# Optimization experiments

Measured on AMD Instinct MI355X. Metric: run time of the kernel, lower is better.

Reference implementation:

```python
import jax, jax.numpy as jnp
import numpy as np

B, T, C = 2, 1024, 1024
NH, HS, BD, HORIZON = 16, 64, 16, 64


def setup_inputs() -> dict:
    key = jax.random.key(0)
    ks = jax.random.split(key, 16)
    s = 0.02
    return {
        "x": jax.random.normal(ks[0], (B, T, C), jnp.float32),
        "W_disp": jax.random.normal(ks[1], (NH * BD, C), jnp.float32) * s,
        "b_disp": jnp.zeros((NH * BD,), jnp.float32),
        "W_val": jax.random.normal(ks[2], (C, C), jnp.float32) * s,
        "b_val": jnp.zeros((C,), jnp.float32),
        "rel_pos_emb": jax.random.normal(ks[3], (HORIZON, BD), jnp.float32) * s,
        "W_fused": jax.random.normal(ks[4], (2 * BD, BD), jnp.float32) * s,
        "b_fused": jnp.zeros((2 * BD,), jnp.float32),
        "W_pos": jax.random.normal(ks[5], (BD, BD), jnp.float32) * s,
        "W_bond": jax.random.normal(ks[6], (BD,), jnp.float32) * s,
        "b_bond": jnp.zeros((), jnp.float32),
        "W_dmg": jax.random.normal(ks[7], (BD,), jnp.float32) * s,
        "b_dmg": jnp.full((), -3.0, jnp.float32),  # nn.init.constant_(damage_out.bias, -3.0)
        "W_cproj": jax.random.normal(ks[8], (C, C), jnp.float32) * s,
        "b_cproj": jnp.zeros((C,), jnp.float32),
    }


def reference(x, W_disp, b_disp, W_val, b_val, rel_pos_emb, W_fused, b_fused,
              W_pos, W_bond, b_bond, W_dmg, b_dmg, W_cproj, b_cproj):
    delta = min(HORIZON, T)
    gelu = lambda z: jax.nn.gelu(z, approximate=False)  # torch F.gelu default (erf)

    # projections + head split: (B,nh,T,bd) / (B,nh,T,hs)
    disp = (x @ W_disp.T + b_disp).reshape(B, T, NH, BD).transpose(0, 2, 1, 3)
    val = (x @ W_val.T + b_val).reshape(B, T, NH, HS).transpose(0, 2, 1, 3)

    pad = delta - 1
    disp_pad = jnp.pad(disp, ((0, 0), (0, 0), (pad, 0), (0, 0)))
    idx = jnp.arange(T)[:, None] + jnp.arange(delta)[None, :]  # (T,delta) into padded axis
    disp_win = disp_pad[:, :, idx]                      # (B,nh,T,delta,bd)
    strain = disp_win - disp[:, :, :, None, :]          # bond strain

    fused = strain @ W_fused.T + b_fused                # (B,nh,T,delta,2bd)
    bond_f, dmg_f = fused[..., :BD], fused[..., BD:]
    pos_feat = rel_pos_emb[:delta] @ W_pos.T            # (delta,bd)

    bond_logits = gelu(bond_f + pos_feat) @ W_bond + b_bond          # (B,nh,T,delta)
    damage = jax.nn.sigmoid(gelu(dmg_f) @ W_dmg + b_dmg)             # (B,nh,T,delta)
    logits = bond_logits - 10.0 * damage

    cmask = (jnp.arange(T)[:, None] - delta + 1 + jnp.arange(delta)[None, :]) >= 0
    logits = jnp.where(cmask[None, None], logits, -jnp.inf)
    weights = jax.nn.softmax(logits, axis=-1)           # (B,nh,T,delta)

    # weighted sum over window without materializing (B,nh,T,delta,hs)
    val_pad = jnp.pad(val, ((0, 0), (0, 0), (pad, 0), (0, 0)))
    def body(acc, j):
        sl = jax.lax.dynamic_slice_in_dim(val_pad, j, T, axis=2)  # (B,nh,T,hs)
        return acc + weights[..., j][..., None] * sl, None
    out0 = jnp.zeros((B, NH, T, HS), jnp.float32)
    out, _ = jax.lax.scan(body, out0, jnp.arange(delta))

    y = out.transpose(0, 2, 1, 3).reshape(B, T, C)
    return y @ W_cproj.T + b_cproj
```

## Files before the change

### kernel.cpp

```cpp
#include <hip/hip_runtime.h>

#define BDIM 16
#define HSZ 64
#define NHEAD 16
#define DELTA 64
#define LOG2E 1.4426950408889634f

typedef __bf16 bf16x8 __attribute__((ext_vector_type(8)));
typedef float f32x4 __attribute__((ext_vector_type(4)));
typedef float f32x2 __attribute__((ext_vector_type(2)));
typedef unsigned short us8 __attribute__((ext_vector_type(8)));
typedef unsigned int u32;

__device__ __forceinline__ unsigned short f2bf(float f) {
    u32 u = __float_as_uint(f);
    return (unsigned short)((u + 0x7fffu + ((u >> 16) & 1u)) >> 16);
}
__device__ __forceinline__ float bf2f(unsigned short s) {
    return __uint_as_float(((u32)s) << 16);
}

__device__ __forceinline__ void gload_lds16(const void* g, void* l) {
    __builtin_amdgcn_global_load_lds(
        (const __attribute__((address_space(1))) void*)g,
        (__attribute__((address_space(3))) void*)l, 16, 0, 0);
}

__global__ __launch_bounds__(256) void cast4_bf16(
    const float* __restrict__ s0, unsigned short* __restrict__ d0,
    const float* __restrict__ s1, unsigned short* __restrict__ d1,
    const float* __restrict__ s2, unsigned short* __restrict__ d2,
    const float* __restrict__ s3, unsigned short* __restrict__ d3,
    const float* __restrict__ bd, const float* __restrict__ bv,
    float* __restrict__ bcat) {
    int blk = blockIdx.x;
    if (blk == 4352) {
        for (int t = threadIdx.x; t < 320; t += 256) {
            if (t < 64) ((float4*)bcat)[t] = ((const float4*)bd)[t];
            else        ((float4*)bcat)[t] = ((const float4*)bv)[t - 64];
        }
        return;
    }
    const float* src; unsigned short* dst; int base;
    if (blk < 2048)      { src = s0; dst = d0; base = blk; }
    else if (blk < 2304) { src = s1; dst = d1; base = blk - 2048; }
    else if (blk < 3328) { src = s2; dst = d2; base = blk - 2304; }
    else                 { src = s3; dst = d3; base = blk - 3328; }
    int i = base * 256 + threadIdx.x;
    float4 f = ((const float4*)src)[i];
    ushort4 o;
    o.x = f2bf(f.x); o.y = f2bf(f.y); o.z = f2bf(f.z); o.w = f2bf(f.w);
    ((ushort4*)dst)[i] = o;
}

__global__ __launch_bounds__(256) void gemm_bf16(const unsigned short* __restrict__ A,
                                                 const unsigned short* __restrict__ Bw,
                                                 const float* __restrict__ bias,
                                                 float* __restrict__ C,
                                                 unsigned short* __restrict__ CbT,
                                                 int N, int K, int nbx, int mode) {
    __shared__ __align__(16) unsigned short lA[2][16 * 512];
    __shared__ __align__(16) unsigned short lB[2][8 * 512];
    int tid = threadIdx.x;
    int w = tid >> 6, lane = tid & 63;
    int id = blockIdx.x;
    int xcd = id & 7, rr = id >> 3;
    int mi = xcd * 2 + (rr & 1);
    int ni = rr >> 1;
    int bm = mi * 128, bn = ni * 64;
    int wr = w & 1, wc = w >> 1;
    int m16 = lane & 15, q = lane >> 4;

    const unsigned short* aPtr[4];
    const unsigned short* bPtr[2];
#pragma unroll
    for (int i = 0; i < 4; ++i) {
        int g = w + 4 * i;
        aPtr[i] = A + (long)(bm + (g & 7) * 16 + m16) * K + (g >> 3) * 32 + q * 8;
    }
#pragma unroll
    for (int i = 0; i < 2; ++i) {
        int g = w + 4 * i;
        bPtr[i] = Bw + (long)(bn + (g & 3) * 16 + m16) * K + (g >> 2) * 32 + q * 8;
    }

    f32x4 acc[4][2];
#pragma unroll
    for (int i = 0; i < 4; ++i)
#pragma unroll
        for (int j = 0; j < 2; ++j) acc[i][j] = (f32x4){0.f, 0.f, 0.f, 0.f};

    int nk = K >> 6;
#pragma unroll
    for (int i = 0; i < 4; ++i) gload_lds16(aPtr[i], &lA[0][(w + 4 * i) * 512]);
#pragma unroll
    for (int i = 0; i < 2; ++i) gload_lds16(bPtr[i], &lB[0][(w + 4 * i) * 512]);

    for (int kt = 0; kt < nk; ++kt) {
        int p = kt & 1;
        __syncthreads();
        if (kt + 1 < nk) {
            int ko = (kt + 1) * 64;
#pragma unroll
            for (int i = 0; i < 4; ++i)
                gload_lds16(aPtr[i] + ko, &lA[p ^ 1][(w + 4 * i) * 512]);
#pragma unroll
            for (int i = 0; i < 2; ++i)
                gload_lds16(bPtr[i] + ko, &lB[p ^ 1][(w + 4 * i) * 512]);
        }
#pragma unroll
        for (int s = 0; s < 2; ++s) {
            bf16x8 af[4], bg[2];
#pragma unroll
            for (int r = 0; r < 4; ++r)
                af[r] = *(const bf16x8*)&lA[p][(s * 8 + wr * 4 + r) * 512 + lane * 8];
#pragma unroll
            for (int n = 0; n < 2; ++n)
                bg[n] = *(const bf16x8*)&lB[p][(s * 4 + wc * 2 + n) * 512 + lane * 8];
#pragma unroll
            for (int r = 0; r < 4; ++r)
#pragma unroll
                for (int n = 0; n < 2; ++n)
                    acc[r][n] = __builtin_amdgcn_mfma_f32_16x16x32_bf16(af[r], bg[n], acc[r][n], 0, 0, 0);
        }
    }

    if (mode == 0 || bn < 256) {
        int ldc = (mode == 0) ? N : 256;
#pragma unroll
        for (int n = 0; n < 2; ++n) {
            int col = bn + wc * 32 + n * 16 + m16;
            float bv = bias[col];
#pragma unroll
            for (int r = 0; r < 4; ++r)
#pragma unroll
                for (int e = 0; e < 4; ++e) {
                    int row = bm + wr * 64 + r * 16 + q * 4 + e;
                    C[(long)row * ldc + col] = acc[r][n][e] + bv;
                }
        }
    } else {
        __syncthreads();
        unsigned short* sC = (unsigned short*)&lA[0][0];
#pragma unroll
        for (int n = 0; n < 2; ++n) {
            int col_l = wc * 32 + n * 16 + m16;
            float bv = bias[bn + col_l];
#pragma unroll
            for (int r = 0; r < 4; ++r)
#pragma unroll
                for (int e = 0; e < 4; ++e) {
                    int row_l = wr * 64 + r * 16 + q * 4 + e;
                    sC[row_l * 64 + col_l] = f2bf(acc[r][n][e] + bv);
                }
        }
        __syncthreads();
        long base0 = ((long)(bm >> 10)) * 1048576 + (long)(bn - 256) * 1024 + (bm & 1023);
#pragma unroll
        for (int it = 0; it < 4; ++it) {
            int slot = it * 256 + tid;
            int hs = (slot >> 3) & 63;
            int tc = (slot & 7) * 8 + (slot >> 9) * 64;
            us8 o;
#pragma unroll
            for (int j = 0; j < 8; ++j) o[j] = sC[(tc + j) * 64 + hs];
            *(us8*)&CbT[base0 + (long)hs * 1024 + tc] = o;
        }
    }
}

__device__ __forceinline__ f32x2 gelu2(f32x2 z) {
    f32x2 z2 = z * z;
    f32x2 u = z * (0.7978845608f + 0.0356774081f * z2);
    f32x2 u2 = u * u;
    f32x2 den = 1.f + 0.33333333f * u2;
    f32x2 r;
    r.x = __builtin_amdgcn_rcpf(den.x);
    r.y = __builtin_amdgcn_rcpf(den.y);
    f32x2 th = u * r;
    f32x2 zh = 0.5f * z;
    return zh + zh * th;
}

#define PROJ_LD 36
#define VW_LD 136

__global__ __launch_bounds__(512) void attn_kernel(
    const float* __restrict__ disp,
    const unsigned short* __restrict__ valT,
    const float* __restrict__ rel,
    const float* __restrict__ Wpos,
    const float* __restrict__ Wf,
    const float* __restrict__ bfu,
    const float* __restrict__ Wb,
    const float* __restrict__ bb_p,
    const float* __restrict__ Wd,
    const float* __restrict__ bd_p,
    unsigned short* __restrict__ y,
    int T) {
    __shared__ __align__(16) unsigned short sWd[64 * VW_LD];
    __shared__ __align__(16) float ov[128 * PROJ_LD + 128 * 16 + 512];
    float* sProj = ov;
    float* sDisp = ov + 128 * PROJ_LD;
    float* sWfT  = sDisp + 128 * 16;
    unsigned short* sValT = (unsigned short*)ov;

    int tid = threadIdx.x;
    int ntile = T / 64;
    int t0 = (blockIdx.x % ntile) * 64;
    int bh = blockIdx.x / ntile;
    int b = bh / NHEAD, h = bh % NHEAD;
    int wave = tid >> 6, lane = tid & 63;
    int m16 = lane & 15, q = lane >> 4;

    {
        uint4 z4 = make_uint4(0, 0, 0, 0);
        for (int i = tid; i < 1088; i += 512) ((uint4*)sWd)[i] = z4;
        sWfT[(tid & 15) * 32 + (tid >> 4)] = Wf[tid];
        {
            int r = tid >> 2, qq = tid & 3;
            int ts = t0 + r - 64;
            float4 v = make_float4(0.f, 0.f, 0.f, 0.f);
            if (ts >= 0)
                v = ((const float4*)(disp + ((long)(b * T + ts) * NHEAD + h) * BDIM))[qq];
            *(float4*)&sDisp[r * 16 + qq * 4] = v;
        }
    }
    __syncthreads();
    for (int idx = tid; idx < 128 * 32; idx += 512) {
        int r = idx >> 5, k = idx & 31;
        float a = 0.f;
#pragma unroll
        for (int d = 0; d < 16; ++d) a += sDisp[r * 16 + d] * sWfT[d * 32 + k];
        sProj[r * PROJ_LD + k] = a;
    }

    float relv[16];
#pragma unroll
    for (int e = 0; e < 4; ++e) {
        float4 rr = ((const float4*)rel)[lane * 4 + e];
        relv[e * 4 + 0] = rr.x; relv[e * 4 + 1] = rr.y;
        relv[e * 4 + 2] = rr.z; relv[e * 4 + 3] = rr.w;
    }
    f32x2 pfd[16], wbd[16];
#pragma unroll
    for (int d = 0; d < 16; ++d) {
        float a = 0.f;
#pragma unroll
        for (int e = 0; e < 16; ++e) a += relv[e] * Wpos[d * 16 + e];
        pfd[d].x = a + bfu[d];
        pfd[d].y = bfu[16 + d];
        wbd[d].x = Wb[d];
        wbd[d].y = Wd[d];
    }
    float bbond = *bb_p, bdmg = *bd_p;
    __syncthreads();

    int wbase = wave * 8;
    for (int rr = 0; rr < 8; ++rr) {
        int tl = wbase + rr;
        int rs = tl + 1 + lane;
        int rc = tl + 64;
        bool valid = (t0 + tl + lane - 63) >= 0;
        float cb[16], cd[16], pb[16], pd[16];
        const float* crow = &sProj[rc * PROJ_LD];
        const float* prow = &sProj[rs * PROJ_LD];
#pragma unroll
        for (int qq = 0; qq < 4; ++qq) {
            float4 v1 = *(const float4*)&crow[qq * 4];
            float4 v2 = *(const float4*)&crow[16 + qq * 4];
            float4 v3 = *(const float4*)&prow[qq * 4];
            float4 v4 = *(const float4*)&prow[16 + qq * 4];
            cb[qq*4+0]=v1.x; cb[qq*4+1]=v1.y; cb[qq*4+2]=v1.z; cb[qq*4+3]=v1.w;
            cd[qq*4+0]=v2.x; cd[qq*4+1]=v2.y; cd[qq*4+2]=v2.z; cd[qq*4+3]=v2.w;
            pb[qq*4+0]=v3.x; pb[qq*4+1]=v3.y; pb[qq*4+2]=v3.z; pb[qq*4+3]=v3.w;
            pd[qq*4+0]=v4.x; pd[qq*4+1]=v4.y; pd[qq*4+2]=v4.z; pd[qq*4+3]=v4.w;
        }
        f32x2 acc2 = (f32x2){bbond, bdmg};
#pragma unroll
        for (int k = 0; k < 16; ++k) {
            f32x2 pz, cz;
            pz.x = pb[k]; pz.y = pd[k];
            cz.x = cb[k]; cz.y = cd[k];
            f32x2 z = pz - cz + pfd[k];
            acc2 = acc2 + gelu2(z) * wbd[k];
        }
        float bl = acc2.x, dm = acc2.y;
        float damage = __builtin_amdgcn_rcpf(1.f + __builtin_exp2f(-dm * LOG2E));
        float logit = bl - 10.f * damage;
        float e = valid ? __builtin_exp2f(logit * LOG2E) : 0.f;
        float ssum = e;
#pragma unroll
        for (int off = 32; off >= 1; off >>= 1) ssum += __shfl_xor(ssum, off);
        sWd[tl * VW_LD + rs] = f2bf(e * __builtin_amdgcn_rcpf(ssum));
    }
    __syncthreads();

    {
        int hs = lane;
        long vbase = ((long)(b * NHEAD * HSZ + h * HSZ + hs)) * T + (t0 - 64);
#pragma unroll
        for (int it = 0; it < 2; ++it) {
            int g = wave * 2 + it;
            int ts0 = t0 - 64 + g * 8;
            us8 v = (us8)0;
            if (ts0 >= 0) v = *(const us8*)&valT[vbase + g * 8];
            *(us8*)&sValT[hs * VW_LD + g * 8] = v;
        }
    }
    __syncthreads();

    {
        int mi = wave >> 1;
        int nh = (wave & 1) * 2;
        int kt0 = mi >> 1;
        f32x4 acc[2];
#pragma unroll
        for (int n = 0; n < 2; ++n) acc[n] = (f32x4){0.f, 0.f, 0.f, 0.f};
#pragma unroll
        for (int kk = 0; kk < 3; ++kk) {
            int kt = kt0 + kk;
            bf16x8 a = *(const bf16x8*)&sWd[(mi * 16 + m16) * VW_LD + kt * 32 + q * 8];
#pragma unroll
            for (int n = 0; n < 2; ++n) {
                bf16x8 bv = *(const bf16x8*)&sValT[((nh + n) * 16 + m16) * VW_LD + kt * 32 + q * 8];
                acc[n] = __builtin_amdgcn_mfma_f32_16x16x32_bf16(a, bv, acc[n], 0, 0, 0);
            }
        }
        int trow = t0 + mi * 16 + q * 4;
#pragma unroll
        for (int n = 0; n < 2; ++n) {
            int col = h * HSZ + (nh + n) * 16 + m16;
#pragma unroll
            for (int e = 0; e < 4; ++e)
                y[(long)(b * T + trow + e) * (NHEAD * HSZ) + col] = f2bf(acc[n][e]);
        }
    }
}

extern "C" void kernel_launch(void* const* d_in, const int* in_sizes, int n_in,
                              void* d_out, int out_size, void* d_ws, size_t ws_size,
                              hipStream_t stream) {
    const float* x       = (const float*)d_in[0];
    const float* W_disp  = (const float*)d_in[1];
    const float* b_disp  = (const float*)d_in[2];
    const float* W_val   = (const float*)d_in[3];
    const float* b_val   = (const float*)d_in[4];
    const float* rel     = (const float*)d_in[5];
    const float* W_fused = (const float*)d_in[6];
    const float* b_fused = (const float*)d_in[7];
    const float* W_pos   = (const float*)d_in[8];
    const float* W_bond  = (const float*)d_in[9];
    const float* b_bond  = (const float*)d_in[10];
    const float* W_dmg   = (const float*)d_in[11];
    const float* b_dmg   = (const float*)d_in[12];
    const float* W_cproj = (const float*)d_in[13];
    const float* b_cproj = (const float*)d_in[14];
    float* out = (float*)d_out;
    float* ws  = (float*)d_ws;

    const int B = 2, T = 1024, C = 1024;
    float* disp = ws;
    float* bcat = disp + 524288;
    unsigned short* x_bf  = (unsigned short*)(bcat + 1280);
    unsigned short* valT  = x_bf + 2097152;
    unsigned short* Wcat  = valT + 2097152;
    unsigned short* Wv_bf = Wcat + 262144;
    unsigned short* Wc_bf = Wv_bf + 1048576;
    unsigned short* y_bf  = x_bf;

    cast4_bf16<<<4353, 256, 0, stream>>>(x, x_bf, W_disp, Wcat, W_val, Wv_bf,
                                         W_cproj, Wc_bf, b_disp, b_val, bcat);

    gemm_bf16<<<320, 256, 0, stream>>>(x_bf, Wcat, bcat, disp, valT,
                                       1280, C, 20, 1);
    attn_kernel<<<dim3(B * NHEAD * (T / 64)), 512, 0, stream>>>(
        disp, valT, rel, W_pos, W_fused, b_fused, W_bond, b_bond, W_dmg, b_dmg,
        y_bf, T);
    gemm_bf16<<<256, 256, 0, stream>>>(y_bf, Wc_bf, b_cproj, out, nullptr,
                                       C, C, 16, 0);
}
```

Baseline: 169.2 us.

## Shrink attention tile to 32 rows with 256-thread blocks

Cuts the attention kernel's per-block query tile from 64 to 32 timesteps and halves the block to 256 threads, doubling the grid to 1024 blocks and setting a launch-bounds occupancy hint of 4 blocks. The LDS buffers shrink to a 96-row halo window, and the MFMA work is remapped so every wave runs all three k-tiles. The intent is more blocks in flight and less LDS per block for better occupancy, at the cost of a larger halo-to-tile overhead: 64 halo rows are recomputed for only 32 outputs.

```diff
diff --git a/kernel.cpp b/kernel.cpp
--- a/kernel.cpp
+++ b/kernel.cpp
@@ -15,9 +15,6 @@
 __device__ __forceinline__ unsigned short f2bf(float f) {
     u32 u = __float_as_uint(f);
     return (unsigned short)((u + 0x7fffu + ((u >> 16) & 1u)) >> 16);
-}
-__device__ __forceinline__ float bf2f(unsigned short s) {
-    return __uint_as_float(((u32)s) << 16);
 }
 
 __device__ __forceinline__ void gload_lds16(const void* g, void* l) {
@@ -183,9 +180,9 @@
 }
 
 #define PROJ_LD 36
-#define VW_LD 136
-
-__global__ __launch_bounds__(512) void attn_kernel(
+#define SW_LD 104
+
+__global__ __launch_bounds__(256, 4) void attn_kernel(
     const float* __restrict__ disp,
     const unsigned short* __restrict__ valT,
     const float* __restrict__ rel,
@@ -198,27 +195,27 @@
     const float* __restrict__ bd_p,
     unsigned short* __restrict__ y,
     int T) {
-    __shared__ __align__(16) unsigned short sWd[64 * VW_LD];
-    __shared__ __align__(16) float ov[128 * PROJ_LD + 128 * 16 + 512];
+    __shared__ __align__(16) unsigned short sWd[32 * SW_LD];
+    __shared__ __align__(16) float ov[96 * PROJ_LD + 96 * 16 + 512];
     float* sProj = ov;
-    float* sDisp = ov + 128 * PROJ_LD;
-    float* sWfT  = sDisp + 128 * 16;
+    float* sDisp = ov + 96 * PROJ_LD;
+    float* sWfT  = sDisp + 96 * 16;
     unsigned short* sValT = (unsigned short*)ov;
 
     int tid = threadIdx.x;
-    int ntile = T / 64;
-    int t0 = (blockIdx.x % ntile) * 64;
-    int bh = blockIdx.x / ntile;
-    int b = bh / NHEAD, h = bh % NHEAD;
+    int t0 = (blockIdx.x & 31) * 32;
+    int bh = blockIdx.x >> 5;
+    int b = bh >> 4, h = bh & 15;
     int wave = tid >> 6, lane = tid & 63;
     int m16 = lane & 15, q = lane >> 4;
 
     {
         uint4 z4 = make_uint4(0, 0, 0, 0);
-        for (int i = tid; i < 1088; i += 512) ((uint4*)sWd)[i] = z4;
+        for (int i = tid; i < 416; i += 256) ((uint4*)sWd)[i] = z4;
         sWfT[(tid & 15) * 32 + (tid >> 4)] = Wf[tid];
-        {
-            int r = tid >> 2, qq = tid & 3;
+        { int j = tid + 256; sWfT[(j & 15) * 32 + (j >> 4)] = Wf[j]; }
+        for (int i = tid; i < 384; i += 256) {
+            int r = i >> 2, qq = i & 3;
             int ts = t0 + r - 64;
             float4 v = make_float4(0.f, 0.f, 0.f, 0.f);
             if (ts >= 0)
@@ -227,7 +224,7 @@
         }
     }
     __syncthreads();
-    for (int idx = tid; idx < 128 * 32; idx += 512) {
+    for (int idx = tid; idx < 96 * 32; idx += 256) {
         int r = idx >> 5, k = idx & 31;
         float a = 0.f;
 #pragma unroll
@@ -292,38 +289,32 @@
         float ssum = e;
 #pragma unroll
         for (int off = 32; off >= 1; off >>= 1) ssum += __shfl_xor(ssum, off);
-        sWd[tl * VW_LD + rs] = f2bf(e * __builtin_amdgcn_rcpf(ssum));
+        sWd[tl * SW_LD + rs] = f2bf(e * __builtin_amdgcn_rcpf(ssum));
     }
     __syncthreads();
 
+    for (int i = tid; i < 768; i += 256) {
+        int g = i >> 6, hs = i & 63;
+        int ts0 = t0 - 64 + g * 8;
+        us8 v = (us8)0;
+        if (ts0 >= 0)
+            v = *(const us8*)&valT[((long)(b * NHEAD * HSZ + h * HSZ + hs)) * T + ts0];
+        *(us8*)&sValT[hs * SW_LD + g * 8] = v;
+    }
+    __syncthreads();
+
     {
-        int hs = lane;
-        long vbase = ((long)(b * NHEAD * HSZ + h * HSZ + hs)) * T + (t0 - 64);
-#pragma unroll
-        for (int it = 0; it < 2; ++it) {
-            int g = wave * 2 + it;
-            int ts0 = t0 - 64 + g * 8;
-            us8 v = (us8)0;
-            if (ts0 >= 0) v = *(const us8*)&valT[vbase + g * 8];
-            *(us8*)&sValT[hs * VW_LD + g * 8] = v;
-        }
-    }
-    __syncthreads();
-
-    {
-        int mi = wave >> 1;
-        int nh = (wave & 1) * 2;
-        int kt0 = mi >> 1;
+        int mi = wave & 1;
+        int nh = (wave >> 1) * 2;
         f32x4 acc[2];
 #pragma unroll
         for (int n = 0; n < 2; ++n) acc[n] = (f32x4){0.f, 0.f, 0.f, 0.f};
 #pragma unroll
-        for (int kk = 0; kk < 3; ++kk) {
-            int kt = kt0 + kk;
-            bf16x8 a = *(const bf16x8*)&sWd[(mi * 16 + m16) * VW_LD + kt * 32 + q * 8];
+        for (int kt = 0; kt < 3; ++kt) {
+            bf16x8 a = *(const bf16x8*)&sWd[(mi * 16 + m16) * SW_LD + kt * 32 + q * 8];
 #pragma unroll
             for (int n = 0; n < 2; ++n) {
-                bf16x8 bv = *(const bf16x8*)&sValT[((nh + n) * 16 + m16) * VW_LD + kt * 32 + q * 8];
+                bf16x8 bv = *(const bf16x8*)&sValT[((nh + n) * 16 + m16) * SW_LD + kt * 32 + q * 8];
                 acc[n] = __builtin_amdgcn_mfma_f32_16x16x32_bf16(a, bv, acc[n], 0, 0, 0);
             }
         }
@@ -374,7 +365,7 @@
 
     gemm_bf16<<<320, 256, 0, stream>>>(x_bf, Wcat, bcat, disp, valT,
                                        1280, C, 20, 1);
-    attn_kernel<<<dim3(B * NHEAD * (T / 64)), 512, 0, stream>>>(
+    attn_kernel<<<dim3(B * NHEAD * (T / 32)), 256, 0, stream>>>(
         disp, valT, rel, W_pos, W_fused, b_fused, W_bond, b_bond, W_dmg, b_dmg,
         y_bf, T);
     gemm_bf16<<<256, 256, 0, stream>>>(y_bf, Wc_bf, b_cproj, out, nullptr,
```

After: 169.8 us. About the same (+0.4%).
